# Optimization experiments

Hardware: AMD Instinct MI355X
Metric: run time of the kernel (lower is better)

The kernel has to match this reference:

```python
import jax, jax.numpy as jnp
import numpy as np

B, T, D, H = 64, 1024, 512, 512  # batch, time, input_dim, num_units


def setup_inputs() -> dict:
    key = jax.random.key(0)
    k1, k2 = jax.random.split(key)
    x = jax.random.normal(k1, (B, T, D), dtype=jnp.float32)
    # BasicRNNCell kernel: [input_dim + num_units, num_units]
    W = jax.random.normal(k2, (D + H, H), dtype=jnp.float32) * (1.0 / np.sqrt(D + H))
    b = jnp.zeros((H,), dtype=jnp.float32)
    return {"x": x, "W": W, "b": b}


def reference(x, W, b):
    # tf.nn.dynamic_rnn with BasicRNNCell: h_t = tanh([x_t, h_{t-1}] @ W + b)
    Wx = W[:D]   # [D, H] input->hidden
    Wh = W[D:]   # [H, H] hidden->hidden
    # Precompute the input contribution for all timesteps in one big GEMM.
    xw = jnp.einsum('btd,dh->bth', x, Wx) + b  # [B, T, H]

    def step(h, xw_t):
        h_new = jnp.tanh(xw_t + h @ Wh)
        return h_new, h_new

    h0 = jnp.zeros((x.shape[0], H), dtype=x.dtype)
    _, outs = jax.lax.scan(step, h0, jnp.swapaxes(xw, 0, 1))  # outs: [T, B, H]
    return jnp.swapaxes(outs, 0, 1)  # [B, T, H]
```

## Files before the change

### kernel.cpp

```cpp
#include <hip/hip_runtime.h>
#include <math.h>

#define Bb 64
#define Tt 1024
#define Dd 512
#define Hh 512

#define TM 128
#define TN 128
#define TK 16
#define LDP (TN + 4)

__global__ __launch_bounds__(256) void gemm_xw(const float* __restrict__ x,
                                               const float* __restrict__ W,
                                               const float* __restrict__ bias,
                                               float* __restrict__ out) {
    __shared__ float As[TK][LDP];
    __shared__ float Bs[TK][LDP];

    const int tid = threadIdx.x;
    const int m0 = blockIdx.x * TM;
    const int n0 = blockIdx.y * TN;
    const int tx = tid & 15;
    const int ty = tid >> 4;

    float acc[8][8];
    #pragma unroll
    for (int i = 0; i < 8; i++)
        #pragma unroll
        for (int j = 0; j < 8; j++) acc[i][j] = 0.0f;

    for (int k0 = 0; k0 < Dd; k0 += TK) {
        #pragma unroll
        for (int i = 0; i < 2; i++) {
            const int idx = tid * 2 + i;
            const int r = idx >> 2;
            const int c = idx & 3;
            const float4 av = *(const float4*)(x + (size_t)(m0 + r) * Dd + k0 + c * 4);
            As[c * 4 + 0][r] = av.x;
            As[c * 4 + 1][r] = av.y;
            As[c * 4 + 2][r] = av.z;
            As[c * 4 + 3][r] = av.w;
            const int kk = idx >> 5;
            const int cg = (idx & 31) * 4;
            const float4 bv = *(const float4*)(W + (size_t)(k0 + kk) * Hh + n0 + cg);
            *(float4*)(&Bs[kk][cg]) = bv;
        }
        __syncthreads();

        #pragma unroll
        for (int kk = 0; kk < TK; kk++) {
            float a[8], b[8];
            #pragma unroll
            for (int i = 0; i < 8; i++) a[i] = As[kk][ty * 8 + i];
            #pragma unroll
            for (int j = 0; j < 8; j++) b[j] = Bs[kk][tx * 8 + j];
            #pragma unroll
            for (int i = 0; i < 8; i++)
                #pragma unroll
                for (int j = 0; j < 8; j++) acc[i][j] += a[i] * b[j];
        }
        __syncthreads();
    }

    #pragma unroll
    for (int i = 0; i < 8; i++) {
        const size_t row = (size_t)(m0 + ty * 8 + i) * Hh;
        const int n = n0 + tx * 8;
        float4 v0, v1;
        v0.x = acc[i][0] + bias[n + 0];
        v0.y = acc[i][1] + bias[n + 1];
        v0.z = acc[i][2] + bias[n + 2];
        v0.w = acc[i][3] + bias[n + 3];
        v1.x = acc[i][4] + bias[n + 4];
        v1.y = acc[i][5] + bias[n + 5];
        v1.z = acc[i][6] + bias[n + 6];
        v1.w = acc[i][7] + bias[n + 7];
        *(float4*)(out + row + n) = v0;
        *(float4*)(out + row + n + 4) = v1;
    }
}

__device__ unsigned long long g_hbuf[(size_t)Bb * 2 * Hh];

__global__ __launch_bounds__(1024, 4) void scan_rnn(const float* __restrict__ W,
                                                    float* __restrict__ out) {
    const float* __restrict__ Wh = W + (size_t)Dd * Hh;
    const int r = blockIdx.x & 63;
    const int c = blockIdx.x >> 6;
    const int tid = threadIdx.x;
    const int g = tid & 31;
    const int s = tid >> 5;

    float* rowbase = out + (size_t)r * Tt * Hh;
    unsigned long long* hrow = g_hbuf + (size_t)r * 2 * Hh;

    __shared__ float hs[Hh];
    __shared__ float ps[32][128];
    __shared__ int sdead;

    float4 w4[16];
    {
        const float4* wbase = (const float4*)(Wh + (size_t)(s * 16) * Hh) + (c * 32 + g);
        #pragma unroll
        for (int kk = 0; kk < 16; kk++) w4[kk] = wbase[(size_t)kk * 128];
    }
    #pragma unroll
    for (int kk = 0; kk < 16; kk++)
        asm volatile("" : "+v"(w4[kk].x), "+v"(w4[kk].y), "+v"(w4[kk].z), "+v"(w4[kk].w));

    if (tid < Hh) hs[tid] = 0.0f;
    if (tid == 0) sdead = 0;
    __syncthreads();

    for (int t = 0; t < Tt; t++) {
        float z = 0.0f;
        if (tid < 128) z = rowbase[(size_t)t * Hh + c * 128 + tid];

        float4 acc; acc.x = acc.y = acc.z = acc.w = 0.0f;
        #pragma unroll
        for (int kq = 0; kq < 4; kq++) {
            const float4 hv = *(const float4*)&hs[s * 16 + kq * 4];
            const float4 a0 = w4[kq * 4 + 0];
            const float4 a1 = w4[kq * 4 + 1];
            const float4 a2 = w4[kq * 4 + 2];
            const float4 a3 = w4[kq * 4 + 3];
            acc.x += hv.x * a0.x; acc.y += hv.x * a0.y; acc.z += hv.x * a0.z; acc.w += hv.x * a0.w;
            acc.x += hv.y * a1.x; acc.y += hv.y * a1.y; acc.z += hv.y * a1.z; acc.w += hv.y * a1.w;
            acc.x += hv.z * a2.x; acc.y += hv.z * a2.y; acc.z += hv.z * a2.z; acc.w += hv.z * a2.w;
            acc.x += hv.w * a3.x; acc.y += hv.w * a3.y; acc.z += hv.w * a3.z; acc.w += hv.w * a3.w;
        }
        *(float4*)&ps[s][g * 4] = acc;
        __syncthreads();

        if (tid < 128) {
            #pragma unroll
            for (int q = 0; q < 32; q++) z += ps[q][tid];
            const float hn = tanhf(z);
            if (t < Tt - 1) {
                const unsigned long long pkt =
                    ((unsigned long long)(unsigned)(t + 1) << 32) | __float_as_uint(hn);
                __hip_atomic_store(&hrow[(size_t)(t & 1) * Hh + c * 128 + tid], pkt,
                                   __ATOMIC_RELAXED, __HIP_MEMORY_SCOPE_AGENT);
                hs[c * 128 + tid] = hn;
            }
            rowbase[(size_t)t * Hh + c * 128 + tid] = hn;
        } else if (tid < 512 && t < Tt - 1) {
            const int p = (tid >> 7) - 1;
            const int cp = p + (p >= c ? 1 : 0);
            const int jj = tid & 127;
            unsigned long long* src = &hrow[(size_t)(t & 1) * Hh + cp * 128 + jj];
            const unsigned want = (unsigned)(t + 1);
            if (sdead == 0) {
                unsigned long long v;
                int spins = 0;
                for (;;) {
                    v = __hip_atomic_load(src, __ATOMIC_RELAXED, __HIP_MEMORY_SCOPE_AGENT);
                    if ((unsigned)(v >> 32) == want) break;
                    __builtin_amdgcn_s_sleep(1);
                    if (++spins > (1 << 18)) { sdead = 1; break; }
                }
                hs[cp * 128 + jj] = __uint_as_float((unsigned)v);
            }
        }
        __syncthreads();
    }
}

extern "C" void kernel_launch(void* const* d_in, const int* in_sizes, int n_in,
                              void* d_out, int out_size, void* d_ws, size_t ws_size,
                              hipStream_t stream) {
    const float* x = (const float*)d_in[0];
    const float* W = (const float*)d_in[1];
    const float* b = (const float*)d_in[2];
    float* out = (float*)d_out;
    (void)d_ws; (void)ws_size;

    dim3 ggrid((Bb * Tt) / TM, Hh / TN);
    gemm_xw<<<ggrid, dim3(256), 0, stream>>>(x, W, b, out);
    scan_rnn<<<dim3(256), dim3(1024), 0, stream>>>(W, out);
}
```

Measured before the change: 2.421 ms.

## Keep hidden state in registers via per-warp polling and shuffles, drop second barrier

Each wave now polls the global h packets it needs itself (16 values per 32-lane half) and broadcasts them with shuffles into a per-thread register array. This removes the shared hidden-state buffer and the second __syncthreads per timestep, and double-buffers the partial-sum array so the next step's writes cannot race with readers. In exchange, global polling traffic rises because every wave polls, including its own block's values, and the spin timeout is shortened.

```diff
diff --git a/kernel.cpp b/kernel.cpp
--- a/kernel.cpp
+++ b/kernel.cpp
@@ -95,8 +95,7 @@
     float* rowbase = out + (size_t)r * Tt * Hh;
     unsigned long long* hrow = g_hbuf + (size_t)r * 2 * Hh;
 
-    __shared__ float hs[Hh];
-    __shared__ float ps[32][128];
+    __shared__ float ps[2][32][128];
     __shared__ int sdead;
 
     float4 w4[16];
@@ -109,61 +108,65 @@
     for (int kk = 0; kk < 16; kk++)
         asm volatile("" : "+v"(w4[kk].x), "+v"(w4[kk].y), "+v"(w4[kk].z), "+v"(w4[kk].w));
 
-    if (tid < Hh) hs[tid] = 0.0f;
+    float hw[16];
+    #pragma unroll
+    for (int i = 0; i < 16; i++) hw[i] = 0.0f;
+
     if (tid == 0) sdead = 0;
     __syncthreads();
 
     for (int t = 0; t < Tt; t++) {
-        float z = 0.0f;
-        if (tid < 128) z = rowbase[(size_t)t * Hh + c * 128 + tid];
+        float zpre = 0.0f;
+        if (tid < 128) zpre = rowbase[(size_t)t * Hh + c * 128 + tid];
 
-        float4 acc; acc.x = acc.y = acc.z = acc.w = 0.0f;
+        float ax = 0.0f, ay = 0.0f, az = 0.0f, aw = 0.0f;
         #pragma unroll
-        for (int kq = 0; kq < 4; kq++) {
-            const float4 hv = *(const float4*)&hs[s * 16 + kq * 4];
-            const float4 a0 = w4[kq * 4 + 0];
-            const float4 a1 = w4[kq * 4 + 1];
-            const float4 a2 = w4[kq * 4 + 2];
-            const float4 a3 = w4[kq * 4 + 3];
-            acc.x += hv.x * a0.x; acc.y += hv.x * a0.y; acc.z += hv.x * a0.z; acc.w += hv.x * a0.w;
-            acc.x += hv.y * a1.x; acc.y += hv.y * a1.y; acc.z += hv.y * a1.z; acc.w += hv.y * a1.w;
-            acc.x += hv.z * a2.x; acc.y += hv.z * a2.y; acc.z += hv.z * a2.z; acc.w += hv.z * a2.w;
-            acc.x += hv.w * a3.x; acc.y += hv.w * a3.y; acc.z += hv.w * a3.z; acc.w += hv.w * a3.w;
+        for (int q = 0; q < 16; q++) {
+            const float h = hw[q];
+            const float4 a = w4[q];
+            ax += h * a.x; ay += h * a.y; az += h * a.z; aw += h * a.w;
         }
-        *(float4*)&ps[s][g * 4] = acc;
+        {
+            float4 accv; accv.x = ax; accv.y = ay; accv.z = az; accv.w = aw;
+            *(float4*)&ps[t & 1][s][g * 4] = accv;
+        }
+
         __syncthreads();
+        const int dead = sdead;
 
         if (tid < 128) {
+            float z = zpre;
             #pragma unroll
-            for (int q = 0; q < 32; q++) z += ps[q][tid];
+            for (int q = 0; q < 32; q++) z += ps[t & 1][q][tid];
             const float hn = tanhf(z);
             if (t < Tt - 1) {
                 const unsigned long long pkt =
                     ((unsigned long long)(unsigned)(t + 1) << 32) | __float_as_uint(hn);
                 __hip_atomic_store(&hrow[(size_t)(t & 1) * Hh + c * 128 + tid], pkt,
                                    __ATOMIC_RELAXED, __HIP_MEMORY_SCOPE_AGENT);
-                hs[c * 128 + tid] = hn;
             }
             rowbase[(size_t)t * Hh + c * 128 + tid] = hn;
-        } else if (tid < 512 && t < Tt - 1) {
-            const int p = (tid >> 7) - 1;
-            const int cp = p + (p >= c ? 1 : 0);
-            const int jj = tid & 127;
-            unsigned long long* src = &hrow[(size_t)(t & 1) * Hh + cp * 128 + jj];
-            const unsigned want = (unsigned)(t + 1);
-            if (sdead == 0) {
+        }
+
+        if (t < Tt - 1) {
+            float f = 0.0f;
+            if (g < 16 && !dead) {
+                unsigned long long* src = &hrow[(size_t)(t & 1) * Hh + s * 16 + g];
+                const unsigned want = (unsigned)(t + 1);
                 unsigned long long v;
                 int spins = 0;
                 for (;;) {
                     v = __hip_atomic_load(src, __ATOMIC_RELAXED, __HIP_MEMORY_SCOPE_AGENT);
                     if ((unsigned)(v >> 32) == want) break;
                     __builtin_amdgcn_s_sleep(1);
-                    if (++spins > (1 << 18)) { sdead = 1; break; }
+                    if (++spins > (1 << 14)) { sdead = 1; break; }
                 }
-                hs[cp * 128 + jj] = __uint_as_float((unsigned)v);
+                f = __uint_as_float((unsigned)v);
             }
+            const int base = tid & 32;
+            #pragma unroll
+            for (int i = 0; i < 16; i++) hw[i] = __shfl(f, base + i, 64);
         }
-        __syncthreads();
     }
 }
 
```

New measurement: 2.500 ms. 3.3% more time.
